# Optimization experiments

Measured on AMD Instinct MI355X. Metric: run time of the kernel, lower is better.

## Reference

```python
import jax, jax.numpy as jnp
import numpy as np

VOCAB = 100000; D = 300; F_NUM = 768
M = 64; N = 16
SURF_L = 4; CTX_L = 50; DOC_L = 100; BODY_L = 200
HEADS = 5


def _conv_relu_avg(x, W, b):
    # x: [B, L, D] tokens-embedded; conv1d (valid) + relu + global avgpool -> [B, F]
    y = jax.lax.conv_general_dilated(x.transpose(0, 2, 1), W, (1,), 'VALID',
                                     dimension_numbers=('NCH', 'OIH', 'NCH'))
    return jax.nn.relu(y + b[None, :, None]).mean(axis=2)


def _mha(q, k, v, num_heads=HEADS):
    # split-head scaled dot-product attention (no learned projections), q:[Lq,D] k,v:[Lk,D]
    Lq, Dm = q.shape
    hd = Dm // num_heads
    qh = q.reshape(Lq, num_heads, hd).transpose(1, 0, 2)
    kh = k.reshape(k.shape[0], num_heads, hd).transpose(1, 0, 2)
    vh = v.reshape(v.shape[0], num_heads, hd).transpose(1, 0, 2)
    att = jax.nn.softmax(jnp.einsum('hqd,hkd->hqk', qh, kh) * (1.0 / np.sqrt(hd)), axis=-1)
    out = jnp.einsum('hqk,hkd->hqd', att, vh)
    return out.transpose(1, 0, 2).reshape(Lq, Dm)


def _cos(a, b, eps=1e-6):
    na = jnp.maximum(jnp.sqrt((a * a).sum(-1)), eps)
    nb = jnp.maximum(jnp.sqrt((b * b).sum(-1)), eps)
    return (a * b).sum(-1) / (na * nb)


def setup_inputs() -> dict:
    key = jax.random.key(0)
    ks = jax.random.split(key, 20)
    inp = {}
    inp['mention_entity'] = jnp.ones((M, N), dtype=jnp.int32)
    inp['m'] = M
    inp['n'] = N
    inp['mention_vec'] = jax.random.randint(ks[0], (M, SURF_L), 0, VOCAB)
    inp['context_vec'] = jax.random.randint(ks[1], (M, CTX_L), 0, VOCAB)
    inp['doc_vec'] = jax.random.randint(ks[2], (DOC_L,), 0, VOCAB)
    inp['title_vec'] = jax.random.normal(ks[3], (N, F_NUM), dtype=jnp.float32)
    inp['body_vec'] = jax.random.randint(ks[4], (N, BODY_L), 0, VOCAB)
    inp['sfeats'] = jnp.zeros((N, 1), dtype=jnp.float32)
    inp['m2c_prior'] = jax.random.uniform(ks[5], (N,), dtype=jnp.float32)
    inp['men2cands'] = jax.random.randint(ks[6], (M, N), 0, VOCAB)
    inp['contexts_ids'] = jax.random.randint(ks[7], (M, CTX_L), 0, VOCAB)
    inp['hand_features'] = jax.random.uniform(ks[8], (N, 1), dtype=jnp.float32)
    inp['bert_doc_vec'] = jax.random.normal(ks[9], (1, F_NUM), dtype=jnp.float32)
    # learned parameters
    inp['embed_table'] = jax.random.normal(ks[10], (VOCAB, D), dtype=jnp.float32) * 0.1
    inp['conv_ms_w'] = jax.random.normal(ks[11], (F_NUM, D, 2), dtype=jnp.float32) * 0.05
    inp['conv_ms_b'] = jnp.zeros((F_NUM,), dtype=jnp.float32)
    inp['conv_mc_w'] = jax.random.normal(ks[12], (F_NUM, D, 5), dtype=jnp.float32) * 0.05
    inp['conv_mc_b'] = jnp.zeros((F_NUM,), dtype=jnp.float32)
    inp['layer_local_w'] = jax.random.normal(ks[13], (7,), dtype=jnp.float32) * 0.3
    inp['layer_local_b'] = jnp.zeros((), dtype=jnp.float32)
    inp['att_w1'] = jax.random.normal(ks[14], (600, 300), dtype=jnp.float32) * 0.05
    inp['att_b1'] = jnp.zeros((300,), dtype=jnp.float32)
    inp['att_w2'] = jax.random.normal(ks[15], (300, 1), dtype=jnp.float32) * 0.05
    inp['att_b2'] = jnp.zeros((), dtype=jnp.float32)
    return inp


def reference(mention_entity, m, n, mention_vec, context_vec, doc_vec, title_vec,
              body_vec, sfeats, m2c_prior, men2cands, contexts_ids, hand_features,
              bert_doc_vec, embed_table, conv_ms_w, conv_ms_b, conv_mc_w, conv_mc_b,
              layer_local_w, layer_local_b, att_w1, att_b1, att_w2, att_b2):
    # per-mention conv features (vectorized over all mentions at once)
    ms = _conv_relu_avg(embed_table[mention_vec], conv_ms_w, conv_ms_b)   # [M,768]
    mc = _conv_relu_avg(embed_table[context_vec], conv_mc_w, conv_mc_b)   # [M,768]
    md = bert_doc_vec[0]                                                  # [768]
    doc_emb = embed_table[doc_vec]                                        # [100,300]
    body_emb = embed_table[body_vec]                                      # [N,200,300]

    # per-candidate cross attention doc<->body, max-pooled over query positions
    att_d_b = jax.vmap(lambda b: _mha(doc_emb, b, b).max(axis=0))(body_emb)          # [N,300]
    att_b_d = jax.vmap(lambda b: _mha(b, doc_emb, doc_emb).max(axis=0))(body_emb)    # [N,300]
    comb = jnp.concatenate([att_d_b, att_b_d], axis=-1)                              # [N,600]
    att_score = jax.nn.sigmoid(jax.nn.relu(comb @ att_w1 + att_b1) @ att_w2 + att_b2)[:, 0]  # [N]

    # LocalCtxAttRanker: candidate-vs-context attention score
    ctx_emb = embed_table[contexts_ids]                                   # [M,50,300]
    cand_emb = embed_table[men2cands]                                     # [M,N,300]
    tok = jnp.einsum('mnd,mtd->mnt', cand_emb, ctx_emb)                   # [M,N,50]
    p = jax.nn.softmax(tok.max(axis=1), axis=-1)                          # [M,50]
    ctxv = jnp.einsum('mt,mtd->md', p, ctx_emb)                           # [M,300]
    local_att = jnp.einsum('mnd,md->mn', cand_emb, ctxv)                  # [M,N]

    cos_st = _cos(ms[:, None, :], title_vec[None, :, :])                  # [M,N]
    cos_dt = _cos(md[None, :], title_vec)                                 # [N]
    cos_ct = _cos(mc[:, None, :], title_vec[None, :, :])                  # [M,N]

    Mm = ms.shape[0]
    bc = lambda v: jnp.broadcast_to(v[None, :], (Mm, v.shape[0]))
    # feature order matches torch.cat((hand_fea, prior, localAtt, attScore, C_score))
    feats = jnp.stack([bc(hand_features[:, 0]), bc(m2c_prior), local_att,
                       bc(att_score), cos_st, bc(cos_dt), cos_ct], axis=-1)  # [M,N,7]
    score = feats @ layer_local_w + layer_local_b                         # [M,N]

    # per-mention standardization (unbiased std, as torch.std), softmax and uniform renorm
    mu = score.mean(axis=1, keepdims=True)
    sd = score.std(axis=1, keepdims=True, ddof=1)
    z = (score - mu) / sd
    sm = jax.nn.softmax(z, axis=1)
    zmin = z.min(axis=1, keepdims=True)
    zmax = z.max(axis=1, keepdims=True)
    u = (z + 1.0 - zmin) / (zmax - zmin)
    u = u / u.sum(axis=1, keepdims=True)
    return (z, sm, u)
```

## Files before the change

kernel.cpp:

```cpp
#include <hip/hip_runtime.h>

#define MM 64
#define NN 16
#define DDIM 300
#define FNUM 768
#define SURF_LL 4
#define CTX_LL 50
#define DOC_LL 100
#define BODY_LL 200
#define NHEADS 5
#define HDIM 60

#define GM 2944
#define GK 1536
#define GN 768

typedef unsigned short u16;
typedef unsigned int u32;
typedef __attribute__((ext_vector_type(8))) short short8;
typedef __attribute__((ext_vector_type(4))) float f32x4;

#define OFF_MSG    0
#define OFF_CTX2G  76800
#define OFF_CANDG  1036800
#define OFF_MS     1344000
#define OFF_MC     1393152
#define OFF_PV0    1442304
#define OFF_PV1    1451904
#define OFF_ASC    1471104
#define OFF_LATT   1471120
#define OFF_ABF    1472144
#define OFF_WTMC   (OFF_ABF + GM*GK/2)
#define OFF_WTMS   (OFF_WTMC + GN*GK/2)
#define OFF_P      (OFF_WTMS + 600*768)

__device__ __forceinline__ u16 f2bf(float x) {
  union { float f; u32 u; } v; v.f = x;
  u32 r = v.u + 0x7FFFu + ((v.u >> 16) & 1u);
  return (u16)(r >> 16);
}

__global__ __launch_bounds__(256) void mega_prep_kernel(
    const float* __restrict__ embed,
    const int* __restrict__ mention_vec,
    const int* __restrict__ context_vec,
    const int* __restrict__ contexts_ids,
    const int* __restrict__ men2cands,
    const float* __restrict__ Wmc,
    const float* __restrict__ Wms,
    float* __restrict__ dst, float* __restrict__ mc,
    u32* __restrict__ Abf, u32* __restrict__ WTmc, float* __restrict__ WTms) {
  int bid = blockIdx.x;
  if (bid < 5250) {
    int e = bid * 256 + threadIdx.x;
    int row = e / DDIM;
    int col = e - row * DDIM;
    int tok;
    if (row < 256)       tok = mention_vec[row];
    else if (row < 3456) tok = contexts_ids[row - 256];
    else                 tok = men2cands[row - 3456];
    dst[e] = embed[(size_t)tok * DDIM + col];
  } else if (bid < 5442) {
    mc[(bid - 5250) * 256 + threadIdx.x] = 0.f;
  } else if (bid < 14274) {
    int idx = (bid - 5442) * 256 + threadIdx.x;
    int r = idx / (GK / 2);
    int kp = idx - r * (GK / 2);
    int k = kp * 2;
    int m = r / 46, t = r - m * 46;
    u32 out = 0;
#pragma unroll
    for (int j = 0; j < 2; j++) {
      int kj = k + j;
      u16 h = 0;
      if (kj < 1500) {
        int tap = kj / 300;
        int d = kj - tap * 300;
        int tok = context_vec[m * CTX_LL + t + tap];
        h = f2bf(embed[(size_t)tok * DDIM + d]);
      }
      out |= (u32)h << (16 * j);
    }
    Abf[idx] = out;
  } else if (bid < 16578) {
    int idx = (bid - 14274) * 256 + threadIdx.x;
    int n = idx / (GK / 2);
    int kp = idx - n * (GK / 2);
    int k = kp * 2;
    u32 out = 0;
#pragma unroll
    for (int j = 0; j < 2; j++) {
      int kj = k + j;
      u16 h = 0;
      if (kj < 1500) {
        int tap = kj / 300;
        int d = kj - tap * 300;
        h = f2bf(Wmc[(size_t)n * 1500 + d * 5 + tap]);
      }
      out |= (u32)h << (16 * j);
    }
    WTmc[idx] = out;
  } else {
    int idx = (bid - 16578) * 256 + threadIdx.x;
    int k = idx / FNUM;
    int f = idx - k * FNUM;
    WTms[idx] = Wms[(size_t)f * 600 + k];
  }
}

__global__ __launch_bounds__(256) void conv_gemm_kernel(
    const u16* __restrict__ A,
    const u16* __restrict__ B,
    const float* __restrict__ bias,
    float* __restrict__ mc) {
  int bn = blockIdx.x, bm = blockIdx.y;
  __shared__ u16 As[64][72];
  __shared__ u16 Bs[64][72];
  int tid = threadIdx.x;
  int w = tid >> 6, lane = tid & 63;
  int wr = w >> 1, wc = w & 1;
  int lg = lane >> 4, lm = lane & 15;
  f32x4 acc[2][2];
#pragma unroll
  for (int i = 0; i < 2; i++)
#pragma unroll
    for (int j = 0; j < 2; j++) acc[i][j] = (f32x4)0.f;
  int c0row = tid >> 3, ck = (tid & 7) * 8;
  const u16* Ag = A + (size_t)(bm * 64) * GK;
  const u16* Bg = B + (size_t)(bn * 64) * GK;
  for (int kt = 0; kt < GK / 64; kt++) {
    int k0 = kt * 64;
    uint4 av0 = *(const uint4*)(Ag + (size_t)c0row * GK + k0 + ck);
    uint4 av1 = *(const uint4*)(Ag + (size_t)(c0row + 32) * GK + k0 + ck);
    uint4 bv0 = *(const uint4*)(Bg + (size_t)c0row * GK + k0 + ck);
    uint4 bv1 = *(const uint4*)(Bg + (size_t)(c0row + 32) * GK + k0 + ck);
    __syncthreads();
    *(uint4*)&As[c0row][ck] = av0;
    *(uint4*)&As[c0row + 32][ck] = av1;
    *(uint4*)&Bs[c0row][ck] = bv0;
    *(uint4*)&Bs[c0row + 32][ck] = bv1;
    __syncthreads();
#pragma unroll
    for (int kk = 0; kk < 2; kk++) {
      short8 af0 = *(const short8*)&As[wr * 32 + lm][kk * 32 + lg * 8];
      short8 af1 = *(const short8*)&As[wr * 32 + 16 + lm][kk * 32 + lg * 8];
      short8 bf0 = *(const short8*)&Bs[wc * 32 + lm][kk * 32 + lg * 8];
      short8 bf1 = *(const short8*)&Bs[wc * 32 + 16 + lm][kk * 32 + lg * 8];
      acc[0][0] = __builtin_amdgcn_mfma_f32_16x16x32_bf16(af0, bf0, acc[0][0], 0, 0, 0);
      acc[0][1] = __builtin_amdgcn_mfma_f32_16x16x32_bf16(af0, bf1, acc[0][1], 0, 0, 0);
      acc[1][0] = __builtin_amdgcn_mfma_f32_16x16x32_bf16(af1, bf0, acc[1][0], 0, 0, 0);
      acc[1][1] = __builtin_amdgcn_mfma_f32_16x16x32_bf16(af1, bf1, acc[1][1], 0, 0, 0);
    }
  }
#pragma unroll
  for (int mf = 0; mf < 2; mf++)
#pragma unroll
    for (int nf = 0; nf < 2; nf++) {
      int col = bn * 64 + wc * 32 + nf * 16 + lm;
      float bb = bias[col];
      int base = bm * 64 + wr * 32 + mf * 16 + lg * 4;
      int mcur = base / 46;
      float s = 0.f;
#pragma unroll
      for (int r = 0; r < 4; r++) {
        float v = fmaxf(acc[mf][nf][r] + bb, 0.f) * (1.0f / 46.0f);
        int mm = (base + r) / 46;
        if (mm != mcur) { atomicAdd(&mc[mcur * FNUM + col], s); s = 0.f; mcur = mm; }
        s += v;
      }
      atomicAdd(&mc[mcur * FNUM + col], s);
    }
}

template <int DIR>
__device__ __forceinline__ void scores_body(
    const float* __restrict__ embed, const int* __restrict__ doc_vec,
    const int* __restrict__ body_vec, float* __restrict__ P, int b,
    float* __restrict__ smem) {
  constexpr int Lq = DIR ? 200 : 100;
  constexpr int Lk = DIR ? 100 : 200;
  constexpr int KPL = DIR ? 2 : 4;
  int qt = b / 80;
  int rem = b - qt * 80;
  int n = rem / 5, h = rem - n * 5;
  const int* qids = DIR ? body_vec + n * BODY_LL : doc_vec;
  const int* kids = DIR ? doc_vec : body_vec + n * BODY_LL;
  float* Ks = smem;
  float* Qs = smem + Lk * 61;
  for (int idx = threadIdx.x; idx < Lk * 15; idx += 256) {
    int r = idx / 15, c = idx - r * 15;
    float4 v = *(const float4*)(embed + (size_t)kids[r] * DDIM + h * HDIM + c * 4);
    float* dp = Ks + r * 61 + c * 4;
    dp[0] = v.x; dp[1] = v.y; dp[2] = v.z; dp[3] = v.w;
  }
  for (int idx = threadIdx.x; idx < 32 * 15; idx += 256) {
    int r = idx / 15, c = idx - r * 15;
    int q = qt * 32 + r; if (q >= Lq) q = Lq - 1;
    float4 v = *(const float4*)(embed + (size_t)qids[q] * DDIM + h * HDIM + c * 4);
    float* dp = Qs + r * 61 + c * 4;
    dp[0] = v.x; dp[1] = v.y; dp[2] = v.z; dp[3] = v.w;
  }
  __syncthreads();
  int w = threadIdx.x >> 6, lane = threadIdx.x & 63;
  float acc[8][KPL];
#pragma unroll
  for (int i = 0; i < 8; i++)
#pragma unroll
    for (int j = 0; j < KPL; j++) acc[i][j] = 0.f;
  for (int d = 0; d < HDIM; d++) {
    float kv[KPL];
#pragma unroll
    for (int j = 0; j < KPL; j++) {
      int kk = lane + 64 * j; if (kk >= Lk) kk = Lk - 1;
      kv[j] = Ks[kk * 61 + d];
    }
#pragma unroll
    for (int i = 0; i < 8; i++) {
      float qv = Qs[(w * 8 + i) * 61 + d];
#pragma unroll
      for (int j = 0; j < KPL; j++) acc[i][j] += qv * kv[j];
    }
  }
  const float scale = 0.12909944487358056f;
#pragma unroll
  for (int i = 0; i < 8; i++) {
    int q = qt * 32 + w * 8 + i;
    float mx = -1e30f;
#pragma unroll
    for (int j = 0; j < KPL; j++)
      if (lane + 64 * j < Lk) mx = fmaxf(mx, acc[i][j]);
#pragma unroll
    for (int o = 32; o >= 1; o >>= 1) mx = fmaxf(mx, __shfl_xor(mx, o));
    float mxs = mx * scale;
    float p[KPL];
    float s = 0.f;
#pragma unroll
    for (int j = 0; j < KPL; j++) {
      p[j] = (lane + 64 * j < Lk) ? __expf(acc[i][j] * scale - mxs) : 0.f;
      s += p[j];
    }
#pragma unroll
    for (int o = 32; o >= 1; o >>= 1) s += __shfl_xor(s, o);
    float inv = 1.0f / s;
    if (q < Lq) {
      float* rowp = P + (size_t)((n * 2 + DIR) * NHEADS + h) * 20000 + q * Lk;
#pragma unroll
      for (int j = 0; j < KPL; j++) {
        int kk = lane + 64 * j;
        if (kk < Lk) rowp[kk] = p[j] * inv;
      }
    }
  }
}

__global__ __launch_bounds__(256) void scores0_kernel(
    const float* __restrict__ embed,
    const int* __restrict__ doc_vec,
    const int* __restrict__ body_vec,
    float* __restrict__ P) {
  __shared__ float smem[(200 + 32) * 61];
  scores_body<0>(embed, doc_vec, body_vec, P, blockIdx.x, smem);
}

__device__ __forceinline__ void conv_ms_body(
    const float* __restrict__ msg, const float* __restrict__ WT,
    const float* __restrict__ B, float* __restrict__ ms, int b) {
  int m = b / 3, fi = b - m * 3;
  int f = fi * 256 + threadIdx.x;
  const float* x = msg + m * SURF_LL * DDIM;
  float a0 = 0.f, a1 = 0.f, a2 = 0.f;
  for (int d = 0; d < DDIM; d++) {
    float v0 = x[d], v1 = x[DDIM + d], v2 = x[2 * DDIM + d], v3 = x[3 * DDIM + d];
    float wA = WT[(size_t)(2 * d) * FNUM + f];
    float wB = WT[(size_t)(2 * d + 1) * FNUM + f];
    a0 += v0 * wA + v1 * wB;
    a1 += v1 * wA + v2 * wB;
    a2 += v2 * wA + v3 * wB;
  }
  float bb = B[f];
  float r = fmaxf(a0 + bb, 0.f) + fmaxf(a1 + bb, 0.f) + fmaxf(a2 + bb, 0.f);
  ms[m * FNUM + f] = r * (1.0f / 3.0f);
}

__device__ __forceinline__ void tokctxv_body(
    const float* __restrict__ candg, const float* __restrict__ ctx2g,
    float* __restrict__ local_att, int m, float* __restrict__ smem) {
  float* ctx   = smem;
  float* tokb  = smem + 4800;
  float* tkmx  = smem + 5072;
  float* pp    = smem + 5136;
  float* sctxv = smem + 5200;
  int tid = threadIdx.x;
  int nI = tid >> 4, tt = tid & 15;
  const float4* ca = (const float4*)(candg + (size_t)(m * NN + nI) * DDIM);
  for (int tile = 0; tile < 4; tile++) {
    int cbase = tile * 16;
    __syncthreads();
    for (int i = tid; i < 16 * DDIM; i += 256) {
      int rr = i / DDIM, cc = i - rr * DDIM;
      int t = cbase + rr;
      ctx[rr * DDIM + cc] = (t < CTX_LL) ? ctx2g[(size_t)(m * CTX_LL + t) * DDIM + cc] : 0.f;
    }
    __syncthreads();
    const float4* cb = (const float4*)(ctx + tt * DDIM);
    float dsum = 0.f;
#pragma unroll
    for (int c = 0; c < 75; c++) {
      float4 a = ca[c], b = cb[c];
      dsum += a.x * b.x + a.y * b.y + a.z * b.z + a.w * b.w;
    }
    tokb[nI * 17 + tt] = dsum;
    __syncthreads();
    if (tid < 16) {
      float mx = -1e30f;
      for (int nn = 0; nn < NN; nn++) mx = fmaxf(mx, tokb[nn * 17 + tid]);
      int t = cbase + tid;
      if (t < CTX_LL) tkmx[t] = mx;
    }
  }
  __syncthreads();
  if (tid < 64) {
    float v = (tid < CTX_LL) ? tkmx[tid] : -1e30f;
    float mx = v;
#pragma unroll
    for (int o = 32; o >= 1; o >>= 1) mx = fmaxf(mx, __shfl_xor(mx, o));
    float e = (tid < CTX_LL) ? expf(v - mx) : 0.f;
    float s = e;
#pragma unroll
    for (int o = 32; o >= 1; o >>= 1) s += __shfl_xor(s, o);
    pp[tid] = e / s;
  }
  __syncthreads();
  for (int d = tid; d < DDIM; d += 256) {
    float acc = 0.f;
    for (int t = 0; t < CTX_LL; t++)
      acc += pp[t] * ctx2g[(size_t)(m * CTX_LL + t) * DDIM + d];
    sctxv[d] = acc;
  }
  __syncthreads();
  int j = tid & 15;
  const float* crow = candg + (size_t)(m * NN + nI) * DDIM;
  float dd = 0.f;
  for (int i = j; i < DDIM; i += 16) dd += crow[i] * sctxv[i];
#pragma unroll
  for (int o = 8; o >= 1; o >>= 1) dd += __shfl_xor(dd, o);
  if (j == 0) local_att[m * NN + nI] = dd;
}

__global__ __launch_bounds__(256) void mega_mid_kernel(
    const float* __restrict__ embed,
    const int* __restrict__ doc_vec,
    const int* __restrict__ body_vec,
    const float* __restrict__ msg,
    const float* __restrict__ WTms,
    const float* __restrict__ Bms,
    const float* __restrict__ candg,
    const float* __restrict__ ctx2g,
    float* __restrict__ ms,
    float* __restrict__ P,
    float* __restrict__ local_att) {
  __shared__ float smem[(100 + 32) * 61];
  int bid = blockIdx.x;
  if (bid < 64) {
    tokctxv_body(candg, ctx2g, local_att, bid, smem);
  } else if (bid < 624) {
    scores_body<1>(embed, doc_vec, body_vec, P, bid - 64, smem);
  } else {
    conv_ms_body(msg, WTms, Bms, ms, bid - 624);
  }
}

__global__ __launch_bounds__(256) void attn_pv_kernel(
    const float* __restrict__ embed,
    const int* __restrict__ doc_vec,
    const int* __restrict__ body_vec,
    const float* __restrict__ P,
    float* __restrict__ pv0,
    float* __restrict__ pv1) {
  int bid = blockIdx.x;
  int dir, pt, n, h;
  if (bid < 160) { dir = 0; h = bid % 5; n = (bid / 5) % 16; pt = bid / 80; }
  else { int b = bid - 160; dir = 1; h = b % 5; n = (b / 5) % 16; pt = b / 80; }
  int Lq = dir ? 200 : 100;
  int Lk = dir ? 100 : 200;
  int Lk4 = Lk >> 2;
  int K4STR = dir ? 27 : 51;
  const int* kids = dir ? doc_vec : body_vec + n * BODY_LL;
  __shared__ float4 Kt4[60 * 51];
  __shared__ float red[4][64];
  float* Ktf = (float*)Kt4;
  int RS = K4STR * 4;
  for (int idx = threadIdx.x; idx < Lk * 15; idx += 256) {
    int r = idx / 15, c = idx - r * 15;
    float4 v = *(const float4*)(embed + (size_t)kids[r] * DDIM + h * HDIM + c * 4);
    Ktf[(c * 4 + 0) * RS + r] = v.x;
    Ktf[(c * 4 + 1) * RS + r] = v.y;
    Ktf[(c * 4 + 2) * RS + r] = v.z;
    Ktf[(c * 4 + 3) * RS + r] = v.w;
  }
  __syncthreads();
  int lane = threadIdx.x & 63;
  int w = __builtin_amdgcn_readfirstlane(threadIdx.x >> 6);
  int dl = (lane < HDIM) ? lane : (HDIM - 1);
  const float4* Krow = Kt4 + dl * K4STR;
  const float* Pb = P + (size_t)((n * 2 + dir) * NHEADS + h) * 20000;
  float omax = -1e30f;
#pragma unroll
  for (int p = 0; p < 4; p++) {
    int q0 = pt * 64 + p * 16 + w * 4;
    int qa0 = min(q0, Lq - 1), qa1 = min(q0 + 1, Lq - 1);
    int qa2 = min(q0 + 2, Lq - 1), qa3 = min(q0 + 3, Lq - 1);
    const float4* P0 = (const float4*)(Pb + (size_t)qa0 * Lk);
    const float4* P1 = (const float4*)(Pb + (size_t)qa1 * Lk);
    const float4* P2 = (const float4*)(Pb + (size_t)qa2 * Lk);
    const float4* P3 = (const float4*)(Pb + (size_t)qa3 * Lk);
    float o0 = 0.f, o1 = 0.f, o2 = 0.f, o3 = 0.f;
    for (int k4 = 0; k4 < Lk4; k4++) {
      float4 pp0 = P0[k4], pp1 = P1[k4], pp2 = P2[k4], pp3 = P3[k4];
      float4 kk = Krow[k4];
      o0 += pp0.x * kk.x + pp0.y * kk.y + pp0.z * kk.z + pp0.w * kk.w;
      o1 += pp1.x * kk.x + pp1.y * kk.y + pp1.z * kk.z + pp1.w * kk.w;
      o2 += pp2.x * kk.x + pp2.y * kk.y + pp2.z * kk.z + pp2.w * kk.w;
      o3 += pp3.x * kk.x + pp3.y * kk.y + pp3.z * kk.z + pp3.w * kk.w;
    }
    if (q0 < Lq)     omax = fmaxf(omax, o0);
    if (q0 + 1 < Lq) omax = fmaxf(omax, o1);
    if (q0 + 2 < Lq) omax = fmaxf(omax, o2);
    if (q0 + 3 < Lq) omax = fmaxf(omax, o3);
  }
  red[threadIdx.x >> 6][lane] = omax;
  __syncthreads();
  if (threadIdx.x < 64 && lane < HDIM) {
    float m4 = fmaxf(fmaxf(red[0][lane], red[1][lane]),
                     fmaxf(red[2][lane], red[3][lane]));
    float* dst = dir ? pv1 + (size_t)((n * NHEADS + h) * 4 + pt) * HDIM
                     : pv0 + (size_t)((n * NHEADS + h) * 2 + pt) * HDIM;
    dst[lane] = m4;
  }
}

__global__ __launch_bounds__(256) void mlp_kernel(
    const float* __restrict__ pv0, const float* __restrict__ pv1,
    const float* __restrict__ w1, const float* __restrict__ b1,
    const float* __restrict__ w2, const float* __restrict__ b2,
    float* __restrict__ att_score) {
  int n = blockIdx.x, tid = threadIdx.x;
  __shared__ float comb[600];
  for (int idx = tid; idx < 300; idx += 256) {
    int h = idx / 60, d = idx - h * 60;
    float mx = -1e30f;
#pragma unroll
    for (int pt = 0; pt < 2; pt++)
      mx = fmaxf(mx, pv0[(size_t)((n * NHEADS + h) * 2 + pt) * HDIM + d]);
    comb[idx] = mx;
    mx = -1e30f;
#pragma unroll
    for (int pt = 0; pt < 4; pt++)
      mx = fmaxf(mx, pv1[(size_t)((n * NHEADS + h) * 4 + pt) * HDIM + d]);
    comb[300 + idx] = mx;
  }
  __syncthreads();
  float partial = 0.f;
  for (int j = tid; j < 300; j += 256) {
    float hh = b1[j];
    for (int k = 0; k < 600; k++) hh += comb[k] * w1[k * 300 + j];
    partial += fmaxf(hh, 0.f) * w2[j];
  }
  __shared__ float redd[256];
  redd[tid] = partial;
  __syncthreads();
  for (int s = 128; s > 0; s >>= 1) {
    if (tid < s) redd[tid] += redd[tid + s];
    __syncthreads();
  }
  if (tid == 0) att_score[n] = 1.0f / (1.0f + expf(-(redd[0] + b2[0])));
}

__global__ __launch_bounds__(256) void final_kernel(
    const float* __restrict__ ms,
    const float* __restrict__ mc,
    const float* __restrict__ title,
    const float* __restrict__ bert,
    const float* __restrict__ att_score,
    const float* __restrict__ m2c_prior,
    const float* __restrict__ hand,
    const float* __restrict__ local_att,
    const float* __restrict__ w7,
    const float* __restrict__ b7,
    float* __restrict__ out) {
  int m = blockIdx.x, tid = threadIdx.x;
  __shared__ float sms[FNUM], smc[FNUM], smd[FNUM];
  __shared__ float snorm[3], sscore[16], wred[3][4];
  for (int i = tid; i < FNUM; i += 256) {
    sms[i] = ms[m * FNUM + i];
    smc[i] = mc[m * FNUM + i];
    smd[i] = bert[i];
  }
  __syncthreads();
  float p1 = 0.f, p2 = 0.f, p3 = 0.f;
  for (int i = tid; i < FNUM; i += 256) {
    float a = sms[i], b = smc[i], c = smd[i];
    p1 += a * a; p2 += b * b; p3 += c * c;
  }
#pragma unroll
  for (int o = 32; o >= 1; o >>= 1) {
    p1 += __shfl_xor(p1, o); p2 += __shfl_xor(p2, o); p3 += __shfl_xor(p3, o);
  }
  int wid = tid >> 6, lane = tid & 63;
  if (lane == 0) { wred[0][wid] = p1; wred[1][wid] = p2; wred[2][wid] = p3; }
  __syncthreads();
  if (tid == 0) {
    snorm[0] = fmaxf(sqrtf(wred[0][0] + wred[0][1] + wred[0][2] + wred[0][3]), 1e-6f);
    snorm[1] = fmaxf(sqrtf(wred[1][0] + wred[1][1] + wred[1][2] + wred[1][3]), 1e-6f);
    snorm[2] = fmaxf(sqrtf(wred[2][0] + wred[2][1] + wred[2][2] + wred[2][3]), 1e-6f);
  }
  __syncthreads();
  int nI = tid >> 4, j = tid & 15;
  float d1 = 0.f, d2 = 0.f, d3 = 0.f, d4 = 0.f;
  for (int i = j; i < FNUM; i += 16) {
    float t = title[nI * FNUM + i];
    d1 += sms[i] * t; d2 += smc[i] * t; d3 += smd[i] * t; d4 += t * t;
  }
#pragma unroll
  for (int o = 8; o >= 1; o >>= 1) {
    d1 += __shfl_xor(d1, o); d2 += __shfl_xor(d2, o);
    d3 += __shfl_xor(d3, o); d4 += __shfl_xor(d4, o);
  }
  if (j == 0) {
    float nt = fmaxf(sqrtf(d4), 1e-6f);
    float cos_st = d1 / (snorm[0] * nt);
    float cos_ct = d2 / (snorm[1] * nt);
    float cos_dt = d3 / (snorm[2] * nt);
    float score = hand[nI] * w7[0] + m2c_prior[nI] * w7[1] +
                  local_att[m * NN + nI] * w7[2] + att_score[nI] * w7[3] +
                  cos_st * w7[4] + cos_dt * w7[5] + cos_ct * w7[6] + b7[0];
    sscore[nI] = score;
  }
  __syncthreads();
  if (tid < 16) {
    float x = sscore[tid];
    float s = x;
#pragma unroll
    for (int o = 8; o >= 1; o >>= 1) s += __shfl_xor(s, o);
    float mu = s * (1.0f / 16.0f);
    float dv = (x - mu) * (x - mu);
    float vs = dv;
#pragma unroll
    for (int o = 8; o >= 1; o >>= 1) vs += __shfl_xor(vs, o);
    float sd = sqrtf(vs * (1.0f / 15.0f));
    float z = (x - mu) / sd;
    float zm = z;
#pragma unroll
    for (int o = 8; o >= 1; o >>= 1) zm = fmaxf(zm, __shfl_xor(zm, o));
    float e = expf(z - zm);
    float es = e;
#pragma unroll
    for (int o = 8; o >= 1; o >>= 1) es += __shfl_xor(es, o);
    float sm = e / es;
    float zmin = z;
#pragma unroll
    for (int o = 8; o >= 1; o >>= 1) zmin = fminf(zmin, __shfl_xor(zmin, o));
    float u0 = (z + 1.0f - zmin) / (zm - zmin);
    float us = u0;
#pragma unroll
    for (int o = 8; o >= 1; o >>= 1) us += __shfl_xor(us, o);
    float u = u0 / us;
    out[m * NN + tid] = z;
    out[MM * NN + m * NN + tid] = sm;
    out[2 * MM * NN + m * NN + tid] = u;
  }
}

extern "C" void kernel_launch(void* const* d_in, const int* in_sizes, int n_in,
                              void* d_out, int out_size, void* d_ws, size_t ws_size,
                              hipStream_t stream) {
  const int*   mention_vec   = (const int*)d_in[3];
  const int*   context_vec   = (const int*)d_in[4];
  const int*   doc_vec       = (const int*)d_in[5];
  const float* title_vec     = (const float*)d_in[6];
  const int*   body_vec      = (const int*)d_in[7];
  const float* m2c_prior     = (const float*)d_in[9];
  const int*   men2cands     = (const int*)d_in[10];
  const int*   contexts_ids  = (const int*)d_in[11];
  const float* hand_features = (const float*)d_in[12];
  const float* bert_doc_vec  = (const float*)d_in[13];
  const float* embed_table   = (const float*)d_in[14];
  const float* conv_ms_w     = (const float*)d_in[15];
  const float* conv_ms_b     = (const float*)d_in[16];
  const float* conv_mc_w     = (const float*)d_in[17];
  const float* conv_mc_b     = (const float*)d_in[18];
  const float* layer_local_w = (const float*)d_in[19];
  const float* layer_local_b = (const float*)d_in[20];
  const float* att_w1        = (const float*)d_in[21];
  const float* att_b1        = (const float*)d_in[22];
  const float* att_w2        = (const float*)d_in[23];
  const float* att_b2        = (const float*)d_in[24];

  float* ws     = (float*)d_ws;
  float* msg    = ws + OFF_MSG;
  float* ctx2g  = ws + OFF_CTX2G;
  float* candg  = ws + OFF_CANDG;
  float* ms     = ws + OFF_MS;
  float* mc     = ws + OFF_MC;
  float* pv0    = ws + OFF_PV0;
  float* pv1    = ws + OFF_PV1;
  float* att_sc = ws + OFF_ASC;
  float* latt   = ws + OFF_LATT;
  u16*   Abf    = (u16*)(ws + OFF_ABF);
  u16*   WTmc   = (u16*)(ws + OFF_WTMC);
  float* WTms   = ws + OFF_WTMS;
  float* P      = ws + OFF_P;
  float* out    = (float*)d_out;

  mega_prep_kernel<<<dim3(18378), dim3(256), 0, stream>>>(
      embed_table, mention_vec, context_vec, contexts_ids, men2cands,
      conv_mc_w, conv_ms_w, ws, mc, (u32*)Abf, (u32*)WTmc, WTms);
  conv_gemm_kernel<<<dim3(GN / 64, GM / 64), dim3(256), 0, stream>>>(
      Abf, WTmc, conv_mc_b, mc);
  scores0_kernel<<<dim3(320), dim3(256), 0, stream>>>(
      embed_table, doc_vec, body_vec, P);
  mega_mid_kernel<<<dim3(816), dim3(256), 0, stream>>>(
      embed_table, doc_vec, body_vec, msg, WTms, conv_ms_b, candg, ctx2g,
      ms, P, latt);
  attn_pv_kernel<<<dim3(480), dim3(256), 0, stream>>>(
      embed_table, doc_vec, body_vec, P, pv0, pv1);
  mlp_kernel<<<dim3(NN), dim3(256), 0, stream>>>(pv0, pv1, att_w1, att_b1, att_w2, att_b2, att_sc);
  final_kernel<<<dim3(MM), dim3(256), 0, stream>>>(
      ms, mc, title_vec, bert_doc_vec, att_sc, m2c_prior, hand_features,
      latt, layer_local_w, layer_local_b, out);
}
```

Before: 437.0 us.

## Fold direction-0 attention scores into mid megakernel with chunked key staging

Removes the separate scores0 kernel launch by adding its blocks to mega_mid_kernel. The direction-0 score computation now stages its 200 keys through shared memory in two 100-row chunks, so it fits the smaller shared buffer of the mid kernel. This saves one launch and lets the score blocks run alongside the other mid-stage work. In exchange it adds an extra sync and reload pass per block, and the shared-memory footprint stays at the mid kernel's size.

```diff
diff --git a/kernel.cpp b/kernel.cpp
--- a/kernel.cpp
+++ b/kernel.cpp
@@ -172,21 +172,18 @@
     }
 }
 
-template <int DIR>
-__device__ __forceinline__ void scores_body(
+__device__ __forceinline__ void scores1_body(
     const float* __restrict__ embed, const int* __restrict__ doc_vec,
     const int* __restrict__ body_vec, float* __restrict__ P, int b,
     float* __restrict__ smem) {
-  constexpr int Lq = DIR ? 200 : 100;
-  constexpr int Lk = DIR ? 100 : 200;
-  constexpr int KPL = DIR ? 2 : 4;
+  constexpr int Lq = 200, Lk = 100, KPL = 2;
   int qt = b / 80;
   int rem = b - qt * 80;
   int n = rem / 5, h = rem - n * 5;
-  const int* qids = DIR ? body_vec + n * BODY_LL : doc_vec;
-  const int* kids = DIR ? doc_vec : body_vec + n * BODY_LL;
+  const int* qids = body_vec + n * BODY_LL;
+  const int* kids = doc_vec;
   float* Ks = smem;
-  float* Qs = smem + Lk * 61;
+  float* Qs = smem + 100 * 61;
   for (int idx = threadIdx.x; idx < Lk * 15; idx += 256) {
     int r = idx / 15, c = idx - r * 15;
     float4 v = *(const float4*)(embed + (size_t)kids[r] * DDIM + h * HDIM + c * 4);
@@ -243,7 +240,7 @@
     for (int o = 32; o >= 1; o >>= 1) s += __shfl_xor(s, o);
     float inv = 1.0f / s;
     if (q < Lq) {
-      float* rowp = P + (size_t)((n * 2 + DIR) * NHEADS + h) * 20000 + q * Lk;
+      float* rowp = P + (size_t)((n * 2 + 1) * NHEADS + h) * 20000 + q * Lk;
 #pragma unroll
       for (int j = 0; j < KPL; j++) {
         int kk = lane + 64 * j;
@@ -253,13 +250,80 @@
   }
 }
 
-__global__ __launch_bounds__(256) void scores0_kernel(
-    const float* __restrict__ embed,
-    const int* __restrict__ doc_vec,
-    const int* __restrict__ body_vec,
-    float* __restrict__ P) {
-  __shared__ float smem[(200 + 32) * 61];
-  scores_body<0>(embed, doc_vec, body_vec, P, blockIdx.x, smem);
+__device__ __forceinline__ void scores0_body(
+    const float* __restrict__ embed, const int* __restrict__ doc_vec,
+    const int* __restrict__ body_vec, float* __restrict__ P, int b,
+    float* __restrict__ smem) {
+  constexpr int Lq = 100, Lk = 200;
+  int qt = b / 80;
+  int rem = b - qt * 80;
+  int n = rem / 5, h = rem - n * 5;
+  const int* qids = doc_vec;
+  const int* kids = body_vec + n * BODY_LL;
+  float* Ks = smem;
+  float* Qs = smem + 100 * 61;
+  for (int idx = threadIdx.x; idx < 32 * 15; idx += 256) {
+    int r = idx / 15, c = idx - r * 15;
+    int q = qt * 32 + r; if (q >= Lq) q = Lq - 1;
+    float4 v = *(const float4*)(embed + (size_t)qids[q] * DDIM + h * HDIM + c * 4);
+    float* dp = Qs + r * 61 + c * 4;
+    dp[0] = v.x; dp[1] = v.y; dp[2] = v.z; dp[3] = v.w;
+  }
+  int w = threadIdx.x >> 6, lane = threadIdx.x & 63;
+  int k1 = (lane < 36) ? (64 + lane) : 99;
+  float acc[8][4];
+#pragma unroll
+  for (int i = 0; i < 8; i++)
+#pragma unroll
+    for (int j = 0; j < 4; j++) acc[i][j] = 0.f;
+  for (int p = 0; p < 2; p++) {
+    __syncthreads();
+    for (int idx = threadIdx.x; idx < 100 * 15; idx += 256) {
+      int r = idx / 15, c = idx - r * 15;
+      float4 v = *(const float4*)(embed + (size_t)kids[p * 100 + r] * DDIM + h * HDIM + c * 4);
+      float* dp = Ks + r * 61 + c * 4;
+      dp[0] = v.x; dp[1] = v.y; dp[2] = v.z; dp[3] = v.w;
+    }
+    __syncthreads();
+    for (int d = 0; d < HDIM; d++) {
+      float kv0 = Ks[lane * 61 + d];
+      float kv1 = Ks[k1 * 61 + d];
+#pragma unroll
+      for (int i = 0; i < 8; i++) {
+        float qv = Qs[(w * 8 + i) * 61 + d];
+        acc[i][p * 2 + 0] += qv * kv0;
+        acc[i][p * 2 + 1] += qv * kv1;
+      }
+    }
+  }
+  const float scale = 0.12909944487358056f;
+  bool v1 = (lane < 36);
+#pragma unroll
+  for (int i = 0; i < 8; i++) {
+    int q = qt * 32 + w * 8 + i;
+    float mx = fmaxf(acc[i][0], acc[i][2]);
+    if (v1) mx = fmaxf(mx, fmaxf(acc[i][1], acc[i][3]));
+#pragma unroll
+    for (int o = 32; o >= 1; o >>= 1) mx = fmaxf(mx, __shfl_xor(mx, o));
+    float mxs = mx * scale;
+    float p0 = __expf(acc[i][0] * scale - mxs);
+    float p1 = v1 ? __expf(acc[i][1] * scale - mxs) : 0.f;
+    float p2 = __expf(acc[i][2] * scale - mxs);
+    float p3 = v1 ? __expf(acc[i][3] * scale - mxs) : 0.f;
+    float s = p0 + p1 + p2 + p3;
+#pragma unroll
+    for (int o = 32; o >= 1; o >>= 1) s += __shfl_xor(s, o);
+    float inv = 1.0f / s;
+    if (q < Lq) {
+      float* rowp = P + (size_t)((n * 2 + 0) * NHEADS + h) * 20000 + q * Lk;
+      rowp[lane] = p0 * inv;
+      rowp[100 + lane] = p2 * inv;
+      if (v1) {
+        rowp[64 + lane] = p1 * inv;
+        rowp[164 + lane] = p3 * inv;
+      }
+    }
+  }
 }
 
 __device__ __forceinline__ void conv_ms_body(
@@ -363,10 +427,12 @@
   int bid = blockIdx.x;
   if (bid < 64) {
     tokctxv_body(candg, ctx2g, local_att, bid, smem);
-  } else if (bid < 624) {
-    scores_body<1>(embed, doc_vec, body_vec, P, bid - 64, smem);
+  } else if (bid < 384) {
+    scores0_body(embed, doc_vec, body_vec, P, bid - 64, smem);
+  } else if (bid < 944) {
+    scores1_body(embed, doc_vec, body_vec, P, bid - 384, smem);
   } else {
-    conv_ms_body(msg, WTms, Bms, ms, bid - 624);
+    conv_ms_body(msg, WTms, Bms, ms, bid - 944);
   }
 }
 
@@ -617,9 +683,7 @@
       conv_mc_w, conv_ms_w, ws, mc, (u32*)Abf, (u32*)WTmc, WTms);
   conv_gemm_kernel<<<dim3(GN / 64, GM / 64), dim3(256), 0, stream>>>(
       Abf, WTmc, conv_mc_b, mc);
-  scores0_kernel<<<dim3(320), dim3(256), 0, stream>>>(
-      embed_table, doc_vec, body_vec, P);
-  mega_mid_kernel<<<dim3(816), dim3(256), 0, stream>>>(
+  mega_mid_kernel<<<dim3(1136), dim3(256), 0, stream>>>(
       embed_table, doc_vec, body_vec, msg, WTms, conv_ms_b, candg, ctx2g,
       ms, P, latt);
   attn_pv_kernel<<<dim3(480), dim3(256), 0, stream>>>(
```

After: 438.2 us. No clear change (+0.3%).
